# Kernel optimization log

Hardware: AMD Instinct MI355X
Metric: run time of the kernel (lower is better)

Reference implementation:

```python
import jax, jax.numpy as jnp
import numpy as np

D_MODEL, N_HEADS, N_KV, HEAD_DIM, D_LAT = 1024, 8, 2, 128, 32
N_REP = N_HEADS // N_KV  # 4
B, T = 2, 2048


def setup_inputs() -> dict:
    key = jax.random.key(0)
    ks = jax.random.split(key, 8)
    s = lambda fan_in: 1.0 / np.sqrt(fan_in)
    return {
        "x": jax.random.normal(ks[0], (B, T, D_MODEL), jnp.float32),
        # weights stored as [in, out] (transpose of torch Linear.weight)
        "wq": jax.random.normal(ks[1], (D_MODEL, N_HEADS * HEAD_DIM), jnp.float32) * s(D_MODEL),
        "wk_down": jax.random.normal(ks[2], (D_MODEL, N_KV * D_LAT), jnp.float32) * s(D_MODEL),
        "wv_down": jax.random.normal(ks[3], (D_MODEL, N_KV * D_LAT), jnp.float32) * s(D_MODEL),
        "wk_up": jax.random.normal(ks[4], (D_LAT, HEAD_DIM), jnp.float32) * s(D_LAT),
        "wv_up": jax.random.normal(ks[5], (D_LAT, HEAD_DIM), jnp.float32) * s(D_LAT),
        "wo": jax.random.normal(ks[6], (N_HEADS * HEAD_DIM, D_MODEL), jnp.float32) * s(N_HEADS * HEAD_DIM),
    }


def reference(x, wq, wk_down, wv_down, wk_up, wv_up, wo):
    Bq, Tq, _ = x.shape
    scale = HEAD_DIM ** -0.5  # SDPA default scale
    # Q: [B,T,Hkv,Rep,Dh] (grouped view avoids materializing repeated K/V)
    q = (x @ wq).reshape(Bq, Tq, N_KV, N_REP, HEAD_DIM)
    # latent KV: [B,T,Hkv,Dl] -> up-project to [B,T,Hkv,Dh]
    k_lat = (x @ wk_down).reshape(Bq, Tq, N_KV, D_LAT)
    v_lat = (x @ wv_down).reshape(Bq, Tq, N_KV, D_LAT)
    k = jnp.einsum("bkhl,ld->bkhd", k_lat, wk_up)
    v = jnp.einsum("bkhl,ld->bkhd", v_lat, wv_up)
    # causal attention, GQA via grouped einsum (no repeat_interleave copy)
    scores = jnp.einsum("bqhrd,bkhd->bhrqk", q, k) * scale  # [B,Hkv,Rep,T,T]
    causal = jnp.tril(jnp.ones((Tq, Tq), dtype=bool))
    scores = jnp.where(causal, scores, jnp.finfo(scores.dtype).min)
    probs = jax.nn.softmax(scores, axis=-1)
    y = jnp.einsum("bhrqk,bkhd->bqhrd", probs, v)  # [B,T,Hkv,Rep,Dh]
    y = y.reshape(Bq, Tq, N_HEADS * HEAD_DIM)
    return y @ wo
```

## Files before the change

kernel.cpp:

```cpp
#include <hip/hip_runtime.h>
#include <hip/hip_bf16.h>


typedef __bf16 bf16_t;
typedef bf16_t bf16x8 __attribute__((ext_vector_type(8)));
typedef float f32x4 __attribute__((ext_vector_type(4)));

__device__ inline bf16x8 cvt8(const float* __restrict__ p) {
  f32x4 a = *(const f32x4*)p, b = *(const f32x4*)(p + 4);
  bf16x8 r;
#pragma unroll
  for (int i = 0; i < 4; ++i) { r[i] = (bf16_t)a[i]; r[4 + i] = (bf16_t)b[i]; }
  return r;
}

__global__ __launch_bounds__(256) void prep_mfma(
    const float* __restrict__ wq, const float* __restrict__ wkd,
    const float* __restrict__ wvd, const float* __restrict__ wku,
    const float* __restrict__ wvu, const float* __restrict__ wo,
    bf16_t* __restrict__ WqkvT, bf16_t* __restrict__ WcombT) {
  __shared__ __align__(16) char smem[34816];
  const int tid = threadIdx.x;
  const int wave = tid >> 6, lane = tid & 63;
  const int quad = lane >> 4, col = lane & 15;
  const int bi = blockIdx.x;

  if (bi < 64) {
    const int h = bi >> 3;
    const int c0 = (bi & 7) * 128 + wave * 32;
    f32x4 acc[2][2];
#pragma unroll
    for (int i = 0; i < 2; ++i)
#pragma unroll
      for (int j = 0; j < 2; ++j) acc[i][j] = (f32x4){0.f, 0.f, 0.f, 0.f};
#pragma unroll
    for (int ks = 0; ks < 4; ++ks) {
      const int ko = ks * 32 + quad * 8;
      bf16x8 a0 = cvt8(wku + col * 128 + ko);
      bf16x8 a1 = cvt8(wku + (16 + col) * 128 + ko);
      bf16x8 b0 = cvt8(wq + (size_t)(c0 + col) * 1024 + h * 128 + ko);
      bf16x8 b1 = cvt8(wq + (size_t)(c0 + 16 + col) * 1024 + h * 128 + ko);
      acc[0][0] = __builtin_amdgcn_mfma_f32_16x16x32_bf16(a0, b0, acc[0][0], 0, 0, 0);
      acc[0][1] = __builtin_amdgcn_mfma_f32_16x16x32_bf16(a0, b1, acc[0][1], 0, 0, 0);
      acc[1][0] = __builtin_amdgcn_mfma_f32_16x16x32_bf16(a1, b0, acc[1][0], 0, 0, 0);
      acc[1][1] = __builtin_amdgcn_mfma_f32_16x16x32_bf16(a1, b1, acc[1][1], 0, 0, 0);
    }
#pragma unroll
    for (int ms = 0; ms < 2; ++ms)
#pragma unroll
      for (int ns = 0; ns < 2; ++ns)
#pragma unroll
        for (int v = 0; v < 4; ++v)
          WqkvT[(size_t)(h * 32 + ms * 16 + quad * 4 + v) * 1024 + c0 + ns * 16 + col] =
              (bf16_t)acc[ms][ns][v];
  } else if (bi < 128) {
    const int b2 = bi - 64;
    const int h = b2 >> 3, m0 = (b2 & 7) * 128;
    bf16_t(*B_lds)[136] = (bf16_t(*)[136])smem;
    {
      const int d = tid >> 1, mh = (tid & 1) * 64;
      const float* wp = wo + (size_t)(h * 128 + d) * 1024 + m0 + mh;
#pragma unroll
      for (int i = 0; i < 16; ++i) {
        f32x4 w4 = *(const f32x4*)(wp + i * 4);
#pragma unroll
        for (int t = 0; t < 4; ++t) B_lds[mh + i * 4 + t][d] = (bf16_t)w4[t];
      }
    }
    __syncthreads();
    f32x4 acc[2][2];
#pragma unroll
    for (int i = 0; i < 2; ++i)
#pragma unroll
      for (int j = 0; j < 2; ++j) acc[i][j] = (f32x4){0.f, 0.f, 0.f, 0.f};
#pragma unroll
    for (int ks = 0; ks < 4; ++ks) {
      const int ko = ks * 32 + quad * 8;
      bf16x8 a0 = cvt8(wvu + col * 128 + ko);
      bf16x8 a1 = cvt8(wvu + (16 + col) * 128 + ko);
      bf16x8 b0 = *(const bf16x8*)&B_lds[wave * 32 + col][ko];
      bf16x8 b1 = *(const bf16x8*)&B_lds[wave * 32 + 16 + col][ko];
      acc[0][0] = __builtin_amdgcn_mfma_f32_16x16x32_bf16(a0, b0, acc[0][0], 0, 0, 0);
      acc[0][1] = __builtin_amdgcn_mfma_f32_16x16x32_bf16(a0, b1, acc[0][1], 0, 0, 0);
      acc[1][0] = __builtin_amdgcn_mfma_f32_16x16x32_bf16(a1, b0, acc[1][0], 0, 0, 0);
      acc[1][1] = __builtin_amdgcn_mfma_f32_16x16x32_bf16(a1, b1, acc[1][1], 0, 0, 0);
    }
#pragma unroll
    for (int ms = 0; ms < 2; ++ms)
#pragma unroll
      for (int ns = 0; ns < 2; ++ns)
#pragma unroll
        for (int v = 0; v < 4; ++v)
          WcombT[(size_t)(m0 + wave * 32 + ns * 16 + col) * 256 +
                 h * 32 + ms * 16 + quad * 4 + v] = (bf16_t)acc[ms][ns][v];
  } else {
    const int b3 = bi - 128;
    const int mat = b3 >> 4, c0 = (b3 & 15) * 64;
    const float* in = mat ? wvd : wkd;
    bf16_t(*tT)[72] = (bf16_t(*)[72])smem;
    {
      const int cc = tid >> 2, jq = (tid & 3) * 16;
      const float* ip = in + (size_t)(c0 + cc) * 64 + jq;
#pragma unroll
      for (int q = 0; q < 4; ++q) {
        f32x4 v4 = *(const f32x4*)(ip + q * 4);
#pragma unroll
        for (int t = 0; t < 4; ++t) tT[jq + q * 4 + t][cc] = (bf16_t)v4[t];
      }
    }
    __syncthreads();
    {
      const int j = tid >> 2, cq = (tid & 3) * 16;
      bf16_t* op = WqkvT + (size_t)(256 + mat * 64 + j) * 1024 + c0 + cq;
      *(bf16x8*)op = *(const bf16x8*)&tT[j][cq];
      *(bf16x8*)(op + 8) = *(const bf16x8*)&tT[j][cq + 8];
    }
  }
}

__global__ __launch_bounds__(256) void gemm_qkv(
    const float* __restrict__ A, const bf16_t* __restrict__ Bt,
    bf16_t* __restrict__ C) {
  __shared__ bf16_t As[32][72];
  __shared__ bf16_t Bs[128][72];
  const int tid = threadIdx.x;
  const int wave = tid >> 6, lane = tid & 63;
  const int quad = lane >> 4, col = lane & 15;
  const int wm = (wave >> 1) * 16, wn = (wave & 1) * 64;
  const int m0 = blockIdx.y * 32, n0 = blockIdx.x * 128;

  f32x4 acc[4];
#pragma unroll
  for (int j = 0; j < 4; ++j) acc[j] = (f32x4){0.f, 0.f, 0.f, 0.f};

  const int ar = tid >> 3, ac = (tid & 7) * 8;
  const int br = tid >> 1, bc = (tid & 1) * 32;
  const float* aP = A + (size_t)(m0 + ar) * 1024 + ac;
  const bf16_t* bP = Bt + (size_t)(n0 + br) * 1024 + bc;

  bf16x8 aR0 = cvt8(aP);
  bf16x8 bR0 = *(const bf16x8*)bP, bR1 = *(const bf16x8*)(bP + 8);
  bf16x8 bR2 = *(const bf16x8*)(bP + 16), bR3 = *(const bf16x8*)(bP + 24);

  for (int kt = 0; kt < 16; ++kt) {
    *(bf16x8*)&As[ar][ac] = aR0;
    *(bf16x8*)&Bs[br][bc] = bR0; *(bf16x8*)&Bs[br][bc + 8] = bR1;
    *(bf16x8*)&Bs[br][bc + 16] = bR2; *(bf16x8*)&Bs[br][bc + 24] = bR3;
    __syncthreads();
    if (kt < 15) {
      const int k0 = (kt + 1) * 64;
      aR0 = cvt8(aP + k0);
      bR0 = *(const bf16x8*)(bP + k0); bR1 = *(const bf16x8*)(bP + k0 + 8);
      bR2 = *(const bf16x8*)(bP + k0 + 16); bR3 = *(const bf16x8*)(bP + k0 + 24);
    }
#pragma unroll
    for (int ks = 0; ks < 2; ++ks) {
      bf16x8 af = *(const bf16x8*)&As[wm + col][ks * 32 + quad * 8];
      bf16x8 bfr[4];
#pragma unroll
      for (int j = 0; j < 4; ++j) bfr[j] = *(const bf16x8*)&Bs[wn + j * 16 + col][ks * 32 + quad * 8];
#pragma unroll
      for (int j = 0; j < 4; ++j)
        acc[j] = __builtin_amdgcn_mfma_f32_16x16x32_bf16(af, bfr[j], acc[j], 0, 0, 0);
    }
    __syncthreads();
  }

#pragma unroll
  for (int j = 0; j < 4; ++j) {
    const int cg = n0 + wn + j * 16 + col;
#pragma unroll
    for (int v = 0; v < 4; ++v)
      C[(size_t)(m0 + wm + quad * 4 + v) * 384 + cg] = (bf16_t)acc[j][v];
  }
}

__global__ __launch_bounds__(256) void gemm_out(
    const bf16_t* __restrict__ A, const bf16_t* __restrict__ Bt,
    float* __restrict__ C) {
  __shared__ bf16_t As[64][72];
  __shared__ bf16_t Bs[128][72];
  const int tid = threadIdx.x;
  const int wave = tid >> 6, lane = tid & 63;
  const int quad = lane >> 4, col = lane & 15;
  const int wm = (wave >> 1) * 32, wn = (wave & 1) * 64;
  const int m0 = blockIdx.y * 64, n0 = blockIdx.x * 128;

  f32x4 acc[2][4];
#pragma unroll
  for (int i = 0; i < 2; ++i)
#pragma unroll
    for (int j = 0; j < 4; ++j) acc[i][j] = (f32x4){0.f, 0.f, 0.f, 0.f};

  const int ar = tid >> 2, ac = (tid & 3) * 16;
  const int br = tid >> 1, bc = (tid & 1) * 32;
  const bf16_t* aP = A + (size_t)(m0 + ar) * 384 + ac;
  const bf16_t* bP = Bt + (size_t)(n0 + br) * 256 + bc;

  bf16x8 aR0 = *(const bf16x8*)aP, aR1 = *(const bf16x8*)(aP + 8);
  bf16x8 bR0 = *(const bf16x8*)bP, bR1 = *(const bf16x8*)(bP + 8);
  bf16x8 bR2 = *(const bf16x8*)(bP + 16), bR3 = *(const bf16x8*)(bP + 24);

  for (int kt = 0; kt < 4; ++kt) {
    *(bf16x8*)&As[ar][ac] = aR0; *(bf16x8*)&As[ar][ac + 8] = aR1;
    *(bf16x8*)&Bs[br][bc] = bR0; *(bf16x8*)&Bs[br][bc + 8] = bR1;
    *(bf16x8*)&Bs[br][bc + 16] = bR2; *(bf16x8*)&Bs[br][bc + 24] = bR3;
    __syncthreads();
    if (kt < 3) {
      const int k0 = (kt + 1) * 64;
      aR0 = *(const bf16x8*)(aP + k0); aR1 = *(const bf16x8*)(aP + k0 + 8);
      bR0 = *(const bf16x8*)(bP + k0); bR1 = *(const bf16x8*)(bP + k0 + 8);
      bR2 = *(const bf16x8*)(bP + k0 + 16); bR3 = *(const bf16x8*)(bP + k0 + 24);
    }
#pragma unroll
    for (int ks = 0; ks < 2; ++ks) {
      bf16x8 af[2], bfr[4];
#pragma unroll
      for (int i = 0; i < 2; ++i) af[i] = *(const bf16x8*)&As[wm + i * 16 + col][ks * 32 + quad * 8];
#pragma unroll
      for (int j = 0; j < 4; ++j) bfr[j] = *(const bf16x8*)&Bs[wn + j * 16 + col][ks * 32 + quad * 8];
#pragma unroll
      for (int i = 0; i < 2; ++i)
#pragma unroll
        for (int j = 0; j < 4; ++j)
          acc[i][j] = __builtin_amdgcn_mfma_f32_16x16x32_bf16(af[i], bfr[j], acc[i][j], 0, 0, 0);
    }
    __syncthreads();
  }

#pragma unroll
  for (int i = 0; i < 2; ++i) {
    const int rg = m0 + wm + i * 16 + quad * 4;
#pragma unroll
    for (int j = 0; j < 4; ++j) {
      const int cg = n0 + wn + j * 16 + col;
#pragma unroll
      for (int v = 0; v < 4; ++v)
        C[(size_t)(rg + v) * 1024 + cg] = acc[i][j][v];
    }
  }
}

__global__ __launch_bounds__(256) void attn_lat(bf16_t* QKV) {
  const int bi = blockIdx.x;
  const int half = bi >> 8, rest = bi & 255;
  const int qt = half ? 127 - (rest >> 1) : (rest >> 1);
  const int hkv = rest & 1, b = half;
  const int tid = threadIdx.x;
  const int wave = tid >> 6, lane = tid & 63;
  const int quad = lane >> 4, col = lane & 15;

  __shared__ bf16_t Ks[2][128][40];
  __shared__ bf16_t Vt[2][32][136];
  __shared__ bf16_t Ps[4][16][136];

  const int qb = qt * 16;
  const size_t rowbase = (size_t)b * 2048;
  const int qcol0 = (hkv * 4 + wave) * 32;

  bf16x8 a_q = *(const bf16x8*)(QKV + (rowbase + qb + col) * 384 + qcol0 + quad * 8);

  f32x4 o0 = (f32x4){0.f, 0.f, 0.f, 0.f};
  f32x4 o1 = (f32x4){0.f, 0.f, 0.f, 0.f};
  float lsum[4] = {0.f, 0.f, 0.f, 0.f};

  const int nkt = (qb >> 7) + 1;
  const float scale = 0.08838834764831843f;

  const int kr = tid >> 1, dc = (tid & 1) * 16;
  const bf16_t* kvBase = QKV + (rowbase + kr) * 384 + 256 + hkv * 32 + dc;

  {
    bf16x8 kA = *(const bf16x8*)kvBase, kB = *(const bf16x8*)(kvBase + 8);
    bf16x8 vA = *(const bf16x8*)(kvBase + 64), vB = *(const bf16x8*)(kvBase + 72);
    *(bf16x8*)&Ks[0][kr][dc] = kA;
    *(bf16x8*)&Ks[0][kr][dc + 8] = kB;
#pragma unroll
    for (int t = 0; t < 8; ++t) { Vt[0][dc + t][kr] = vA[t]; Vt[0][dc + 8 + t][kr] = vB[t]; }
  }
  __syncthreads();

  for (int kt = 0; kt < nkt; ++kt) {
    const int cur = kt & 1;
    const int kb = kt * 128;
    const bool more = (kt + 1 < nkt);

    bf16x8 kA, kB, vA, vB;
    if (more) {
      const bf16_t* np = kvBase + (size_t)(kt + 1) * 128 * 384;
      kA = *(const bf16x8*)np; kB = *(const bf16x8*)(np + 8);
      vA = *(const bf16x8*)(np + 64); vB = *(const bf16x8*)(np + 72);
    }

    f32x4 s[8];
#pragma unroll
    for (int k8 = 0; k8 < 8; ++k8) {
      bf16x8 bk = *(const bf16x8*)&Ks[cur][k8 * 16 + col][quad * 8];
      s[k8] = __builtin_amdgcn_mfma_f32_16x16x32_bf16(a_q, bk, (f32x4){0.f, 0.f, 0.f, 0.f}, 0, 0, 0);
    }

    const bool full = (kb + 128 <= qb);
#pragma unroll
    for (int v = 0; v < 4; ++v) {
      const int qr = quad * 4 + v;
      const int qg = qb + qr;
#pragma unroll
      for (int k8 = 0; k8 < 8; ++k8) {
        float xx = s[k8][v] * scale;
        if (!full && (kb + k8 * 16 + col > qg)) xx = -1e30f;
        const float p = __expf(xx);
        lsum[v] += p;
        Ps[wave][qr][k8 * 16 + col] = (bf16_t)p;
      }
    }
    __asm__ __volatile__("" ::: "memory");

#pragma unroll
    for (int kc = 0; kc < 4; ++kc) {
      bf16x8 a_p = *(const bf16x8*)&Ps[wave][col][kc * 32 + quad * 8];
      bf16x8 bv0 = *(const bf16x8*)&Vt[cur][col][kc * 32 + quad * 8];
      bf16x8 bv1 = *(const bf16x8*)&Vt[cur][16 + col][kc * 32 + quad * 8];
      o0 = __builtin_amdgcn_mfma_f32_16x16x32_bf16(a_p, bv0, o0, 0, 0, 0);
      o1 = __builtin_amdgcn_mfma_f32_16x16x32_bf16(a_p, bv1, o1, 0, 0, 0);
    }

    if (more) {
      *(bf16x8*)&Ks[cur ^ 1][kr][dc] = kA;
      *(bf16x8*)&Ks[cur ^ 1][kr][dc + 8] = kB;
#pragma unroll
      for (int t = 0; t < 8; ++t) { Vt[cur ^ 1][dc + t][kr] = vA[t]; Vt[cur ^ 1][dc + 8 + t][kr] = vB[t]; }
    }
    __syncthreads();
  }

#pragma unroll
  for (int v = 0; v < 4; ++v) {
    float l = lsum[v];
#pragma unroll
    for (int off = 8; off; off >>= 1) l += __shfl_xor(l, off, 64);
    const float inv = 1.f / l;
    const size_t r = (rowbase + qb + quad * 4 + v) * 384 + qcol0;
    QKV[r + col] = (bf16_t)(o0[v] * inv);
    QKV[r + 16 + col] = (bf16_t)(o1[v] * inv);
  }
}

extern "C" void kernel_launch(void* const* d_in, const int* in_sizes, int n_in,
                              void* d_out, int out_size, void* d_ws, size_t ws_size,
                              hipStream_t stream) {
  (void)in_sizes; (void)n_in; (void)out_size; (void)ws_size;
  const float* x   = (const float*)d_in[0];
  const float* wq  = (const float*)d_in[1];
  const float* wkd = (const float*)d_in[2];
  const float* wvd = (const float*)d_in[3];
  const float* wku = (const float*)d_in[4];
  const float* wvu = (const float*)d_in[5];
  const float* wo  = (const float*)d_in[6];
  float* out = (float*)d_out;

  bf16_t* WqkvT  = (bf16_t*)d_ws;
  bf16_t* WcombT = WqkvT + (size_t)384 * 1024;
  bf16_t* QKV    = WcombT + (size_t)1024 * 256;

  prep_mfma<<<160, 256, 0, stream>>>(wq, wkd, wvd, wku, wvu, wo, WqkvT, WcombT);
  gemm_qkv<<<dim3(3, 128), 256, 0, stream>>>(x, WqkvT, QKV);
  attn_lat<<<512, 256, 0, stream>>>(QKV);
  gemm_out<<<dim3(8, 64), 256, 0, stream>>>(QKV, WcombT, out);
}
```

Before: 139.5 us.

## Stage Wq via LDS in prep, double GEMM K-tiles, split causal mask branch

Measured after the change: 145.0 us. +3.9%, slower.

```diff
diff --git a/kernel.cpp b/kernel.cpp
--- a/kernel.cpp
+++ b/kernel.cpp
@@ -27,7 +27,20 @@
 
   if (bi < 64) {
     const int h = bi >> 3;
-    const int c0 = (bi & 7) * 128 + wave * 32;
+    const int c0 = (bi & 7) * 128;
+    bf16_t(*Wq)[136] = (bf16_t(*)[136])smem;
+    {
+      const int cc = tid >> 1, dseg = (tid & 1) * 64;
+      const float* wp = wq + (size_t)(c0 + cc) * 1024 + h * 128 + dseg;
+#pragma unroll
+      for (int i = 0; i < 16; ++i) {
+        f32x4 w4 = *(const f32x4*)(wp + i * 4);
+#pragma unroll
+        for (int t = 0; t < 4; ++t) Wq[cc][dseg + i * 4 + t] = (bf16_t)w4[t];
+      }
+    }
+    __syncthreads();
+    const int cw = wave * 32;
     f32x4 acc[2][2];
 #pragma unroll
     for (int i = 0; i < 2; ++i)
@@ -38,8 +51,8 @@
       const int ko = ks * 32 + quad * 8;
       bf16x8 a0 = cvt8(wku + col * 128 + ko);
       bf16x8 a1 = cvt8(wku + (16 + col) * 128 + ko);
-      bf16x8 b0 = cvt8(wq + (size_t)(c0 + col) * 1024 + h * 128 + ko);
-      bf16x8 b1 = cvt8(wq + (size_t)(c0 + 16 + col) * 1024 + h * 128 + ko);
+      bf16x8 b0 = *(const bf16x8*)&Wq[cw + col][ko];
+      bf16x8 b1 = *(const bf16x8*)&Wq[cw + 16 + col][ko];
       acc[0][0] = __builtin_amdgcn_mfma_f32_16x16x32_bf16(a0, b0, acc[0][0], 0, 0, 0);
       acc[0][1] = __builtin_amdgcn_mfma_f32_16x16x32_bf16(a0, b1, acc[0][1], 0, 0, 0);
       acc[1][0] = __builtin_amdgcn_mfma_f32_16x16x32_bf16(a1, b0, acc[1][0], 0, 0, 0);
@@ -51,7 +64,7 @@
       for (int ns = 0; ns < 2; ++ns)
 #pragma unroll
         for (int v = 0; v < 4; ++v)
-          WqkvT[(size_t)(h * 32 + ms * 16 + quad * 4 + v) * 1024 + c0 + ns * 16 + col] =
+          WqkvT[(size_t)(h * 32 + ms * 16 + quad * 4 + v) * 1024 + c0 + cw + ns * 16 + col] =
               (bf16_t)acc[ms][ns][v];
   } else if (bi < 128) {
     const int b2 = bi - 64;
@@ -121,8 +134,8 @@
 __global__ __launch_bounds__(256) void gemm_qkv(
     const float* __restrict__ A, const bf16_t* __restrict__ Bt,
     bf16_t* __restrict__ C) {
-  __shared__ bf16_t As[32][72];
-  __shared__ bf16_t Bs[128][72];
+  __shared__ bf16_t As[32][136];
+  __shared__ bf16_t Bs[128][136];
   const int tid = threadIdx.x;
   const int wave = tid >> 6, lane = tid & 63;
   const int quad = lane >> 4, col = lane & 15;
@@ -133,28 +146,29 @@
 #pragma unroll
   for (int j = 0; j < 4; ++j) acc[j] = (f32x4){0.f, 0.f, 0.f, 0.f};
 
-  const int ar = tid >> 3, ac = (tid & 7) * 8;
-  const int br = tid >> 1, bc = (tid & 1) * 32;
+  const int ar = tid >> 3, ac = (tid & 7) * 16;
+  const int br = tid >> 1, bc = (tid & 1) * 64;
   const float* aP = A + (size_t)(m0 + ar) * 1024 + ac;
   const bf16_t* bP = Bt + (size_t)(n0 + br) * 1024 + bc;
 
-  bf16x8 aR0 = cvt8(aP);
-  bf16x8 bR0 = *(const bf16x8*)bP, bR1 = *(const bf16x8*)(bP + 8);
-  bf16x8 bR2 = *(const bf16x8*)(bP + 16), bR3 = *(const bf16x8*)(bP + 24);
-
-  for (int kt = 0; kt < 16; ++kt) {
-    *(bf16x8*)&As[ar][ac] = aR0;
-    *(bf16x8*)&Bs[br][bc] = bR0; *(bf16x8*)&Bs[br][bc + 8] = bR1;
-    *(bf16x8*)&Bs[br][bc + 16] = bR2; *(bf16x8*)&Bs[br][bc + 24] = bR3;
-    __syncthreads();
-    if (kt < 15) {
-      const int k0 = (kt + 1) * 64;
-      aR0 = cvt8(aP + k0);
-      bR0 = *(const bf16x8*)(bP + k0); bR1 = *(const bf16x8*)(bP + k0 + 8);
-      bR2 = *(const bf16x8*)(bP + k0 + 16); bR3 = *(const bf16x8*)(bP + k0 + 24);
-    }
-#pragma unroll
-    for (int ks = 0; ks < 2; ++ks) {
+  bf16x8 aR[2], bR[8];
+  aR[0] = cvt8(aP); aR[1] = cvt8(aP + 8);
+#pragma unroll
+  for (int t = 0; t < 8; ++t) bR[t] = *(const bf16x8*)(bP + t * 8);
+
+  for (int kt = 0; kt < 8; ++kt) {
+    *(bf16x8*)&As[ar][ac] = aR[0]; *(bf16x8*)&As[ar][ac + 8] = aR[1];
+#pragma unroll
+    for (int t = 0; t < 8; ++t) *(bf16x8*)&Bs[br][bc + t * 8] = bR[t];
+    __syncthreads();
+    if (kt < 7) {
+      const int k0 = (kt + 1) * 128;
+      aR[0] = cvt8(aP + k0); aR[1] = cvt8(aP + k0 + 8);
+#pragma unroll
+      for (int t = 0; t < 8; ++t) bR[t] = *(const bf16x8*)(bP + k0 + t * 8);
+    }
+#pragma unroll
+    for (int ks = 0; ks < 4; ++ks) {
       bf16x8 af = *(const bf16x8*)&As[wm + col][ks * 32 + quad * 8];
       bf16x8 bfr[4];
 #pragma unroll
@@ -178,8 +192,8 @@
 __global__ __launch_bounds__(256) void gemm_out(
     const bf16_t* __restrict__ A, const bf16_t* __restrict__ Bt,
     float* __restrict__ C) {
-  __shared__ bf16_t As[64][72];
-  __shared__ bf16_t Bs[128][72];
+  __shared__ bf16_t As[64][136];
+  __shared__ bf16_t Bs[128][136];
   const int tid = threadIdx.x;
   const int wave = tid >> 6, lane = tid & 63;
   const int quad = lane >> 4, col = lane & 15;
@@ -192,28 +206,31 @@
 #pragma unroll
     for (int j = 0; j < 4; ++j) acc[i][j] = (f32x4){0.f, 0.f, 0.f, 0.f};
 
-  const int ar = tid >> 2, ac = (tid & 3) * 16;
-  const int br = tid >> 1, bc = (tid & 1) * 32;
+  const int ar = tid >> 2, ac = (tid & 3) * 32;
+  const int br = tid >> 1, bc = (tid & 1) * 64;
   const bf16_t* aP = A + (size_t)(m0 + ar) * 384 + ac;
   const bf16_t* bP = Bt + (size_t)(n0 + br) * 256 + bc;
 
-  bf16x8 aR0 = *(const bf16x8*)aP, aR1 = *(const bf16x8*)(aP + 8);
-  bf16x8 bR0 = *(const bf16x8*)bP, bR1 = *(const bf16x8*)(bP + 8);
-  bf16x8 bR2 = *(const bf16x8*)(bP + 16), bR3 = *(const bf16x8*)(bP + 24);
-
-  for (int kt = 0; kt < 4; ++kt) {
-    *(bf16x8*)&As[ar][ac] = aR0; *(bf16x8*)&As[ar][ac + 8] = aR1;
-    *(bf16x8*)&Bs[br][bc] = bR0; *(bf16x8*)&Bs[br][bc + 8] = bR1;
-    *(bf16x8*)&Bs[br][bc + 16] = bR2; *(bf16x8*)&Bs[br][bc + 24] = bR3;
-    __syncthreads();
-    if (kt < 3) {
-      const int k0 = (kt + 1) * 64;
-      aR0 = *(const bf16x8*)(aP + k0); aR1 = *(const bf16x8*)(aP + k0 + 8);
-      bR0 = *(const bf16x8*)(bP + k0); bR1 = *(const bf16x8*)(bP + k0 + 8);
-      bR2 = *(const bf16x8*)(bP + k0 + 16); bR3 = *(const bf16x8*)(bP + k0 + 24);
-    }
-#pragma unroll
-    for (int ks = 0; ks < 2; ++ks) {
+  bf16x8 aR[4], bR[8];
+#pragma unroll
+  for (int t = 0; t < 4; ++t) aR[t] = *(const bf16x8*)(aP + t * 8);
+#pragma unroll
+  for (int t = 0; t < 8; ++t) bR[t] = *(const bf16x8*)(bP + t * 8);
+
+  for (int kt = 0; kt < 2; ++kt) {
+#pragma unroll
+    for (int t = 0; t < 4; ++t) *(bf16x8*)&As[ar][ac + t * 8] = aR[t];
+#pragma unroll
+    for (int t = 0; t < 8; ++t) *(bf16x8*)&Bs[br][bc + t * 8] = bR[t];
+    __syncthreads();
+    if (kt < 1) {
+#pragma unroll
+      for (int t = 0; t < 4; ++t) aR[t] = *(const bf16x8*)(aP + 128 + t * 8);
+#pragma unroll
+      for (int t = 0; t < 8; ++t) bR[t] = *(const bf16x8*)(bP + 128 + t * 8);
+    }
+#pragma unroll
+    for (int ks = 0; ks < 4; ++ks) {
       bf16x8 af[2], bfr[4];
 #pragma unroll
       for (int i = 0; i < 2; ++i) af[i] = *(const bf16x8*)&As[wm + i * 16 + col][ks * 32 + quad * 8];
@@ -299,18 +316,29 @@
       s[k8] = __builtin_amdgcn_mfma_f32_16x16x32_bf16(a_q, bk, (f32x4){0.f, 0.f, 0.f, 0.f}, 0, 0, 0);
     }
 
-    const bool full = (kb + 128 <= qb);
-#pragma unroll
-    for (int v = 0; v < 4; ++v) {
-      const int qr = quad * 4 + v;
-      const int qg = qb + qr;
-#pragma unroll
-      for (int k8 = 0; k8 < 8; ++k8) {
-        float xx = s[k8][v] * scale;
-        if (!full && (kb + k8 * 16 + col > qg)) xx = -1e30f;
-        const float p = __expf(xx);
-        lsum[v] += p;
-        Ps[wave][qr][k8 * 16 + col] = (bf16_t)p;
+    if (kb + 128 <= qb) {
+#pragma unroll
+      for (int v = 0; v < 4; ++v) {
+        const int qr = quad * 4 + v;
+#pragma unroll
+        for (int k8 = 0; k8 < 8; ++k8) {
+          const float p = __expf(s[k8][v] * scale);
+          lsum[v] += p;
+          Ps[wave][qr][k8 * 16 + col] = (bf16_t)p;
+        }
+      }
+    } else {
+#pragma unroll
+      for (int v = 0; v < 4; ++v) {
+        const int qr = quad * 4 + v;
+        const int qg = qb + qr;
+#pragma unroll
+        for (int k8 = 0; k8 < 8; ++k8) {
+          float xx = (kb + k8 * 16 + col <= qg) ? s[k8][v] * scale : -1e30f;
+          const float p = __expf(xx);
+          lsum[v] += p;
+          Ps[wave][qr][k8 * 16 + col] = (bf16_t)p;
+        }
       }
     }
     __asm__ __volatile__("" ::: "memory");
```
